# Optimization experiments

Hardware: AMD Instinct MI355X
Metric: run time of the kernel (lower is better)

Reference implementation:

```python
import jax, jax.numpy as jnp
import numpy as np

N = 30000      # nodes
E = 480000     # directed edges (before self loops)
G = 64         # graphs in batch
L = 20         # padded token-list length per node feature
D = 32         # embedding_dim
S = 64         # scalar_feature_count
H, C = 4, 128  # conv1 heads / hidden_channels
TOT = S + 5 * D  # 224
EPS_LN = 1e-5


def setup_inputs() -> dict:
    key = jax.random.key(0)
    ks = jax.random.split(key, 24)
    f32 = jnp.float32
    rn = lambda k, shp: jax.random.normal(k, shp, dtype=f32) * 0.05
    inp = {}
    inp["x_scalar"] = jax.random.normal(ks[0], (N, S), dtype=f32)
    inp["x_opcode"] = jax.random.randint(ks[1], (N, L), 0, 512)
    inp["x_source"] = jax.random.randint(ks[2], (N, L), 0, 256)
    inp["x_sink"] = jax.random.randint(ks[3], (N, L), 0, 256)
    inp["x_string_manip"] = jax.random.randint(ks[4], (N, L), 0, 128)
    inp["x_payload"] = jax.random.randint(ks[5], (N, L), 0, 256)
    inp["edge_index"] = jax.random.randint(ks[6], (2, E), 0, N)
    inp["batch"] = jnp.sort(jax.random.randint(ks[7], (N,), 0, G))
    inp["emb_opcode"] = rn(ks[8], (512, D))
    inp["emb_source"] = rn(ks[9], (256, D))
    inp["emb_sink"] = rn(ks[10], (256, D))
    inp["emb_string"] = rn(ks[11], (128, D))
    inp["emb_payload"] = rn(ks[12], (256, D))
    inp["ln_scale"] = jnp.ones((TOT,), f32)
    inp["ln_bias"] = jnp.zeros((TOT,), f32)
    inp["W1"] = rn(ks[13], (TOT, H * C))
    inp["att_src1"] = rn(ks[14], (H, C))
    inp["att_dst1"] = rn(ks[15], (H, C))
    inp["b1"] = jnp.zeros((H * C,), f32)
    inp["W2"] = rn(ks[16], (H * C, C))
    inp["att_src2"] = rn(ks[17], (1, C))
    inp["att_dst2"] = rn(ks[18], (1, C))
    inp["b2"] = jnp.zeros((C,), f32)
    return inp


def masked_pool(table, idx):
    # padding_idx=0 masked mean over the list dim
    emb = table[idx]                                    # [N, L, D]
    mask = (idx != 0).astype(emb.dtype)[..., None]      # [N, L, 1]
    return (emb * mask).sum(1) / (mask.sum(1) + 1e-9)   # [N, D]


def layer_norm(x, scale, bias):
    mu = x.mean(-1, keepdims=True)
    var = jnp.mean((x - mu) ** 2, -1, keepdims=True)
    return (x - mu) * jax.lax.rsqrt(var + EPS_LN) * scale + bias


def gat_layer(x, src, dst, W, a_src, a_dst, bias, n):
    # PyG GATConv (eval mode, concat=True, negative_slope=0.2)
    heads, c = a_src.shape
    h = (x @ W).reshape(n, heads, c)                    # [N, H, C]
    s = (h * a_src).sum(-1)                             # [N, H]
    d = (h * a_dst).sum(-1)                             # [N, H]
    e = jax.nn.leaky_relu(s[src] + d[dst], 0.2)         # [E, H]
    m = jax.ops.segment_max(e, dst, num_segments=n)     # segment softmax over dst
    ex = jnp.exp(e - m[dst])
    den = jax.ops.segment_sum(ex, dst, num_segments=n)
    alpha = ex / den[dst]                               # [E, H]
    out = jax.ops.segment_sum(alpha[:, :, None] * h[src], dst, num_segments=n)
    return out.reshape(n, heads * c) + bias


def reference(x_scalar, x_opcode, x_source, x_sink, x_string_manip, x_payload,
              edge_index, batch,
              emb_opcode, emb_source, emb_sink, emb_string, emb_payload,
              ln_scale, ln_bias,
              W1, att_src1, att_dst1, b1,
              W2, att_src2, att_dst2, b2):
    n = x_scalar.shape[0]
    feats = jnp.concatenate([
        x_scalar,
        masked_pool(emb_opcode, x_opcode),
        masked_pool(emb_source, x_source),
        masked_pool(emb_sink, x_sink),
        masked_pool(emb_string, x_string_manip),
        masked_pool(emb_payload, x_payload),
    ], axis=1)
    x = layer_norm(feats, ln_scale, ln_bias)
    # PyG GATConv adds self loops by default
    loops = jnp.arange(n)
    src = jnp.concatenate([edge_index[0], loops])
    dst = jnp.concatenate([edge_index[1], loops])
    x = jax.nn.elu(gat_layer(x, src, dst, W1, att_src1, att_dst1, b1, n))
    x = jax.nn.elu(gat_layer(x, src, dst, W2, att_src2, att_dst2, b2, n))
    # global_max_pool over graphs
    return jax.ops.segment_max(x, batch, num_segments=G)
```

## Files before the change

kernel.cpp:

```cpp
#include <hip/hip_runtime.h>
#include <hip/hip_bf16.h>
#include <math.h>

#define N_NODES 30000
#define M_PAD   30080
#define N_EDGES 480000
#define N_GRAPH 64
#define L_TOK   20
#define D_EMB   32
#define S_SCAL  64
#define TOT     224
#define H1      4
#define C1      128
#define F1      512
#define F2      128
#define E_TOT   (N_EDGES + N_NODES)

typedef __attribute__((ext_vector_type(8))) short bf16x8;
typedef __attribute__((ext_vector_type(4))) float f32x4;

__device__ __forceinline__ unsigned short f2b(float f) {
    unsigned u = __float_as_uint(f);
    u += 0x7FFFu + ((u >> 16) & 1u);
    return (unsigned short)(u >> 16);
}
__device__ __forceinline__ float b2f(unsigned short h) {
    return __uint_as_float(((unsigned)h) << 16);
}
__device__ __forceinline__ float blo(unsigned u) { return __uint_as_float(u << 16); }
__device__ __forceinline__ float bhi(unsigned u) { return __uint_as_float(u & 0xFFFF0000u); }

__device__ __forceinline__ void gload_lds16(const void* g, void* l) {
    __builtin_amdgcn_global_load_lds(
        (const __attribute__((address_space(1))) unsigned int*)g,
        (__attribute__((address_space(3))) unsigned int*)l, 16, 0, 0);
}

__global__ void init_all(int* deg, float* s1, float* d1, float* s2, float* d2) {
    int i = blockIdx.x * blockDim.x + threadIdx.x;
    if (i < N_NODES) {
        deg[i] = 1;
        s2[i] = 0.f; d2[i] = 0.f;
        float4 z = make_float4(0.f, 0.f, 0.f, 0.f);
        *reinterpret_cast<float4*>(&s1[i * 4]) = z;
        *reinterpret_cast<float4*>(&d1[i * 4]) = z;
    }
}

__global__ void add_deg(const int* __restrict__ ei, int* deg) {
    int e = blockIdx.x * blockDim.x + threadIdx.x;
    if (e < N_EDGES) atomicAdd(&deg[ei[N_EDGES + e]], 1);
}

#define SCAN_PER 30
__global__ void scan_deg(const int* __restrict__ deg, int* __restrict__ rowptr,
                         int* __restrict__ cursor) {
    int t = threadIdx.x, lane = t & 63, wid = t >> 6;
    int base = t * SCAN_PER;
    int v[SCAN_PER];
    int lsum = 0;
    #pragma unroll
    for (int i = 0; i < SCAN_PER; ++i) {
        int ii = base + i;
        int d = (ii < N_NODES) ? deg[ii] : 0;
        v[i] = lsum;
        lsum += d;
    }
    int incl = lsum;
    #pragma unroll
    for (int off = 1; off < 64; off <<= 1) {
        int u = __shfl_up(incl, off);
        if (lane >= off) incl += u;
    }
    __shared__ int wsum[16], woff[16];
    if (lane == 63) wsum[wid] = incl;
    __syncthreads();
    if (t == 0) {
        int run = 0;
        #pragma unroll
        for (int w = 0; w < 16; ++w) { woff[w] = run; run += wsum[w]; }
        rowptr[N_NODES] = run;
    }
    __syncthreads();
    int texcl = woff[wid] + (incl - lsum);
    #pragma unroll
    for (int i = 0; i < SCAN_PER; ++i) {
        int ii = base + i;
        if (ii < N_NODES) { int p = texcl + v[i]; rowptr[ii] = p; cursor[ii] = p; }
    }
}

__global__ void scatter_edges(const int* __restrict__ ei, int* cursor, int* csr_src) {
    int e = blockIdx.x * blockDim.x + threadIdx.x;
    if (e < N_EDGES) {
        int src = ei[e], dst = ei[N_EDGES + e];
        int pos = atomicAdd(&cursor[dst], 1);
        csr_src[pos] = src;
    } else if (e < E_TOT) {
        int n = e - N_EDGES;
        int pos = atomicAdd(&cursor[n], 1);
        csr_src[pos] = n;
    }
}

__global__ void transpose_cast2(const float* __restrict__ Wa, unsigned short* __restrict__ WaT,
                                const float* __restrict__ Wb, unsigned short* __restrict__ WbT) {
    __shared__ float tile[32][33];
    int bid = blockIdx.x;
    const float* W; unsigned short* WT; int K, N, kb, nb;
    if (bid < (TOT / 32) * (F1 / 32)) {
        W = Wa; WT = WaT; K = TOT; N = F1;
        kb = (bid % (TOT / 32)) * 32; nb = (bid / (TOT / 32)) * 32;
    } else {
        bid -= (TOT / 32) * (F1 / 32);
        W = Wb; WT = WbT; K = F1; N = F2;
        kb = (bid % (F1 / 32)) * 32; nb = (bid / (F1 / 32)) * 32;
    }
    int t = threadIdx.x;
    int r = t >> 3, c4 = (t & 7) * 4;
    float4 v = *reinterpret_cast<const float4*>(&W[(size_t)(kb + r) * N + nb + c4]);
    tile[r][c4 + 0] = v.x; tile[r][c4 + 1] = v.y;
    tile[r][c4 + 2] = v.z; tile[r][c4 + 3] = v.w;
    __syncthreads();
    ushort4 o;
    o.x = f2b(tile[c4 + 0][r]); o.y = f2b(tile[c4 + 1][r]);
    o.z = f2b(tile[c4 + 2][r]); o.w = f2b(tile[c4 + 3][r]);
    *reinterpret_cast<ushort4*>(&WT[(size_t)(nb + r) * K + kb + c4]) = o;
}

__global__ void feat_ln(const float* __restrict__ xs,
                        const int* __restrict__ xo, const int* __restrict__ xsrc,
                        const int* __restrict__ xsink, const int* __restrict__ xstr,
                        const int* __restrict__ xpay,
                        const float* __restrict__ eo, const float* __restrict__ es,
                        const float* __restrict__ ek, const float* __restrict__ eg,
                        const float* __restrict__ ep,
                        const float* __restrict__ lns, const float* __restrict__ lnb,
                        unsigned short* __restrict__ x0) {
    int node = blockIdx.x * 4 + (threadIdx.x >> 6);
    if (node >= N_NODES) return;
    int lane = threadIdx.x & 63;
    int c = lane * 4;
    float f0 = 0.f, f1 = 0.f, f2 = 0.f, f3 = 0.f;
    if (lane < 16) {
        float4 v = *reinterpret_cast<const float4*>(&xs[(size_t)node * S_SCAL + c]);
        f0 = v.x; f1 = v.y; f2 = v.z; f3 = v.w;
    } else if (lane < 56) {
        int t = c - S_SCAL;
        int ti = t >> 5, dim = t & 31;
        const int* idx; const float* emb;
        switch (ti) {
            case 0: idx = xo;   emb = eo; break;
            case 1: idx = xsrc; emb = es; break;
            case 2: idx = xsink;emb = ek; break;
            case 3: idx = xstr; emb = eg; break;
            default:idx = xpay; emb = ep; break;
        }
        float a0 = 0.f, a1 = 0.f, a2 = 0.f, a3 = 0.f, cnt = 0.f;
        #pragma unroll
        for (int l = 0; l < L_TOK; ++l) {
            int id = idx[node * L_TOK + l];
            if (id != 0) {
                float4 e = *reinterpret_cast<const float4*>(&emb[id * D_EMB + dim]);
                a0 += e.x; a1 += e.y; a2 += e.z; a3 += e.w; cnt += 1.f;
            }
        }
        float r = 1.f / (cnt + 1e-9f);
        f0 = a0 * r; f1 = a1 * r; f2 = a2 * r; f3 = a3 * r;
    }
    float s = f0 + f1 + f2 + f3;
    float q = f0 * f0 + f1 * f1 + f2 * f2 + f3 * f3;
    #pragma unroll
    for (int off = 32; off; off >>= 1) {
        s += __shfl_xor(s, off);
        q += __shfl_xor(q, off);
    }
    float mu = s * (1.f / (float)TOT);
    float var = q * (1.f / (float)TOT) - mu * mu;
    float rs = rsqrtf(var + 1e-5f);
    if (lane < 56) {
        float4 sc = *reinterpret_cast<const float4*>(&lns[c]);
        float4 bi = *reinterpret_cast<const float4*>(&lnb[c]);
        ushort4 o;
        o.x = f2b((f0 - mu) * rs * sc.x + bi.x);
        o.y = f2b((f1 - mu) * rs * sc.y + bi.y);
        o.z = f2b((f2 - mu) * rs * sc.z + bi.z);
        o.w = f2b((f3 - mu) * rs * sc.w + bi.w);
        *reinterpret_cast<ushort4*>(&x0[(size_t)node * TOT + c]) = o;
    }
}

__global__ void gemm_bf16(const unsigned short* __restrict__ A,
                          const unsigned short* __restrict__ BT,
                          unsigned short* __restrict__ C, int M, int N, int K,
                          const float* __restrict__ asrc, const float* __restrict__ adst,
                          float* __restrict__ sOut, float* __restrict__ dOut, int H) {
    __shared__ unsigned short As[128 * 32];
    __shared__ unsigned short Bs[128 * 32];
    int tid = threadIdx.x;
    int w = tid >> 6, lane = tid & 63;
    int l15 = lane & 15, kb = lane >> 4;
    int wr = w >> 1, wc = w & 1;
    int bm = blockIdx.x * 128, bn = blockIdx.y * 128;
    f32x4 acc[4][4] = {};
    int lrow = lane >> 2, lslot = lane & 3;

    for (int k0 = 0; k0 < K; k0 += 32) {
        #pragma unroll
        for (int j = 0; j < 2; ++j) {
            int rbase = w * 16 + j * 64;
            int row = rbase + lrow;
            int scol = (lslot ^ (row & 3)) * 8;
            gload_lds16(&A[(size_t)(bm + row) * K + k0 + scol], &As[rbase * 32]);
            gload_lds16(&BT[(size_t)(bn + row) * K + k0 + scol], &Bs[rbase * 32]);
        }
        __syncthreads();
        bf16x8 af[4], bf[4];
        #pragma unroll
        for (int m = 0; m < 4; ++m) {
            int row = wr * 64 + m * 16 + l15;
            af[m] = *reinterpret_cast<const bf16x8*>(&As[row * 32 + (kb ^ (row & 3)) * 8]);
        }
        #pragma unroll
        for (int n = 0; n < 4; ++n) {
            int row = wc * 64 + n * 16 + l15;
            bf[n] = *reinterpret_cast<const bf16x8*>(&Bs[row * 32 + (kb ^ (row & 3)) * 8]);
        }
        #pragma unroll
        for (int m = 0; m < 4; ++m)
            #pragma unroll
            for (int n = 0; n < 4; ++n)
                acc[m][n] = __builtin_amdgcn_mfma_f32_16x16x32_bf16(af[m], bf[n], acc[m][n], 0, 0, 0);
        __syncthreads();
    }
    #pragma unroll
    for (int m = 0; m < 4; ++m) {
        #pragma unroll
        for (int r = 0; r < 4; ++r) {
            int row = bm + wr * 64 + m * 16 + kb * 4 + r;
            if (row < M) {
                #pragma unroll
                for (int n = 0; n < 4; ++n)
                    C[(size_t)row * N + bn + wc * 64 + n * 16 + l15] = f2b(acc[m][n][r]);
            }
        }
    }
    {
        float a_s[4], a_d[4];
        #pragma unroll
        for (int n = 0; n < 4; ++n) {
            a_s[n] = asrc[bn + wc * 64 + n * 16 + l15];
            a_d[n] = adst[bn + wc * 64 + n * 16 + l15];
        }
        int head = bn / (N / H);
        #pragma unroll
        for (int m = 0; m < 4; ++m) {
            #pragma unroll
            for (int r = 0; r < 4; ++r) {
                float ps = acc[m][0][r] * a_s[0] + acc[m][1][r] * a_s[1]
                         + acc[m][2][r] * a_s[2] + acc[m][3][r] * a_s[3];
                float pd = acc[m][0][r] * a_d[0] + acc[m][1][r] * a_d[1]
                         + acc[m][2][r] * a_d[2] + acc[m][3][r] * a_d[3];
                #pragma unroll
                for (int off = 8; off >= 1; off >>= 1) {
                    ps += __shfl_xor(ps, off);
                    pd += __shfl_xor(pd, off);
                }
                if (l15 == 0) {
                    int row = bm + wr * 64 + m * 16 + kb * 4 + r;
                    if (row < M) {
                        atomicAdd(&sOut[row * H + head], ps);
                        atomicAdd(&dOut[row * H + head], pd);
                    }
                }
            }
        }
    }
}

#define ACC8(v, a) \
    acc[0] += (a) * blo((v).x); acc[1] += (a) * bhi((v).x); \
    acc[2] += (a) * blo((v).y); acc[3] += (a) * bhi((v).y); \
    acc[4] += (a) * blo((v).z); acc[5] += (a) * bhi((v).z); \
    acc[6] += (a) * blo((v).w); acc[7] += (a) * bhi((v).w);

__global__ void gat1_aggregate(const unsigned short* __restrict__ h1, const float* __restrict__ s1,
                               const float* __restrict__ d1, const int* __restrict__ rowptr,
                               const int* __restrict__ csr, const float* __restrict__ b1,
                               unsigned short* __restrict__ x1) {
    int n = blockIdx.x, tid = threadIdx.x;
    int wave = tid >> 6, lane = tid & 63;
    int head = lane >> 4;
    int r0 = rowptr[n], deg = rowptr[n + 1] - r0;
    __shared__ float alpha_sh[H1][68];
    __shared__ int src_sh[64];
    __shared__ float d_n[H1];
    __shared__ float red[3][512];
    if (tid < H1) d_n[tid] = d1[n * H1 + tid];
    __syncthreads();
    float dnw = d_n[wave];
    const uint4* h1u4 = (const uint4*)h1;
    float acc[8] = {};

    auto gather = [&](int cnt) {
        int iA = wave, iB = wave + 4, iC = wave + 8, iD = wave + 12;
        bool hA = iA < cnt, hB = iB < cnt, hC = iC < cnt, hD = iD < cnt;
        int s; float aA, aB, aC, aD; uint4 vA, vB, vC, vD;
        if (hA) { s = __builtin_amdgcn_readfirstlane(src_sh[iA]); aA = alpha_sh[head][iA]; vA = h1u4[(size_t)s * 64 + lane]; }
        if (hB) { s = __builtin_amdgcn_readfirstlane(src_sh[iB]); aB = alpha_sh[head][iB]; vB = h1u4[(size_t)s * 64 + lane]; }
        if (hC) { s = __builtin_amdgcn_readfirstlane(src_sh[iC]); aC = alpha_sh[head][iC]; vC = h1u4[(size_t)s * 64 + lane]; }
        if (hD) { s = __builtin_amdgcn_readfirstlane(src_sh[iD]); aD = alpha_sh[head][iD]; vD = h1u4[(size_t)s * 64 + lane]; }
        while (hA) {
            {
                uint4 v = vA; float a = aA;
                iA += 16; hA = iA < cnt;
                if (hA) { s = __builtin_amdgcn_readfirstlane(src_sh[iA]); aA = alpha_sh[head][iA]; vA = h1u4[(size_t)s * 64 + lane]; }
                ACC8(v, a)
            }
            if (hB) {
                uint4 v = vB; float a = aB;
                iB += 16; hB = iB < cnt;
                if (hB) { s = __builtin_amdgcn_readfirstlane(src_sh[iB]); aB = alpha_sh[head][iB]; vB = h1u4[(size_t)s * 64 + lane]; }
                ACC8(v, a)
            }
            if (hC) {
                uint4 v = vC; float a = aC;
                iC += 16; hC = iC < cnt;
                if (hC) { s = __builtin_amdgcn_readfirstlane(src_sh[iC]); aC = alpha_sh[head][iC]; vC = h1u4[(size_t)s * 64 + lane]; }
                ACC8(v, a)
            }
            if (hD) {
                uint4 v = vD; float a = aD;
                iD += 16; hD = iD < cnt;
                if (hD) { s = __builtin_amdgcn_readfirstlane(src_sh[iD]); aD = alpha_sh[head][iD]; vD = h1u4[(size_t)s * 64 + lane]; }
                ACC8(v, a)
            }
        }
    };

    if (deg <= 64) {
        float e = -1e30f;
        if (lane < deg) {
            int src = csr[r0 + lane];
            if (wave == 0) src_sh[lane] = src;
            float ev = s1[src * H1 + wave] + dnw;
            e = (ev >= 0.f) ? ev : 0.2f * ev;
        }
        float m = e;
        #pragma unroll
        for (int off = 32; off; off >>= 1) m = fmaxf(m, __shfl_xor(m, off));
        float ex = (lane < deg) ? __expf(e - m) : 0.f;
        float den = ex;
        #pragma unroll
        for (int off = 32; off; off >>= 1) den += __shfl_xor(den, off);
        alpha_sh[wave][lane] = ex / den;
        __syncthreads();
        gather(deg);
    } else {
        float m = -1e30f;
        for (int i = lane; i < deg; i += 64) {
            int src = csr[r0 + i];
            float e = s1[src * H1 + wave] + dnw;
            e = (e >= 0.f) ? e : 0.2f * e;
            m = fmaxf(m, e);
        }
        #pragma unroll
        for (int off = 32; off; off >>= 1) m = fmaxf(m, __shfl_xor(m, off));
        float den = 0.f;
        for (int i = lane; i < deg; i += 64) {
            int src = csr[r0 + i];
            float e = s1[src * H1 + wave] + dnw;
            e = (e >= 0.f) ? e : 0.2f * e;
            den += __expf(e - m);
        }
        #pragma unroll
        for (int off = 32; off; off >>= 1) den += __shfl_xor(den, off);
        float invw = 1.f / den;
        for (int c0 = 0; c0 < deg; c0 += 64) {
            __syncthreads();
            int i = c0 + lane;
            if (i < deg) {
                int src = csr[r0 + i];
                if (wave == 0) src_sh[lane] = src;
                float e = s1[src * H1 + wave] + dnw;
                e = (e >= 0.f) ? e : 0.2f * e;
                alpha_sh[wave][lane] = __expf(e - m) * invw;
            }
            __syncthreads();
            gather(min(64, deg - c0));
        }
    }
    if (wave > 0) {
        *reinterpret_cast<float4*>(&red[wave - 1][lane * 4]) =
            make_float4(acc[0], acc[1], acc[2], acc[3]);
        *reinterpret_cast<float4*>(&red[wave - 1][256 + lane * 4]) =
            make_float4(acc[4], acc[5], acc[6], acc[7]);
    }
    __syncthreads();
    if (wave == 0) {
        #pragma unroll
        for (int w = 0; w < 3; ++w) {
            float4 p = *reinterpret_cast<float4*>(&red[w][lane * 4]);
            float4 q = *reinterpret_cast<float4*>(&red[w][256 + lane * 4]);
            acc[0] += p.x; acc[1] += p.y; acc[2] += p.z; acc[3] += p.w;
            acc[4] += q.x; acc[5] += q.y; acc[6] += q.z; acc[7] += q.w;
        }
        float4 b0 = *reinterpret_cast<const float4*>(&b1[lane * 8]);
        float4 b4 = *reinterpret_cast<const float4*>(&b1[lane * 8 + 4]);
        float v0 = acc[0] + b0.x; v0 = (v0 > 0.f) ? v0 : expm1f(v0);
        float v1 = acc[1] + b0.y; v1 = (v1 > 0.f) ? v1 : expm1f(v1);
        float v2 = acc[2] + b0.z; v2 = (v2 > 0.f) ? v2 : expm1f(v2);
        float v3 = acc[3] + b0.w; v3 = (v3 > 0.f) ? v3 : expm1f(v3);
        float v4 = acc[4] + b4.x; v4 = (v4 > 0.f) ? v4 : expm1f(v4);
        float v5 = acc[5] + b4.y; v5 = (v5 > 0.f) ? v5 : expm1f(v5);
        float v6 = acc[6] + b4.z; v6 = (v6 > 0.f) ? v6 : expm1f(v6);
        float v7 = acc[7] + b4.w; v7 = (v7 > 0.f) ? v7 : expm1f(v7);
        uint4 pk;
        pk.x = (unsigned)f2b(v0) | ((unsigned)f2b(v1) << 16);
        pk.y = (unsigned)f2b(v2) | ((unsigned)f2b(v3) << 16);
        pk.z = (unsigned)f2b(v4) | ((unsigned)f2b(v5) << 16);
        pk.w = (unsigned)f2b(v6) | ((unsigned)f2b(v7) << 16);
        ((uint4*)x1)[(size_t)n * 64 + lane] = pk;
    }
}

__global__ void gat2_node(const unsigned short* __restrict__ h2, const float* __restrict__ s2,
                          const float* __restrict__ d2, const int* __restrict__ rowptr,
                          const int* __restrict__ csr, const float* __restrict__ b2,
                          float* __restrict__ h2act) {
    int n = blockIdx.x, tid = threadIdx.x;
    int wid = tid >> 6, lane = tid & 63;
    int grp = tid >> 4, l16 = tid & 15;
    int r0 = rowptr[n], deg = rowptr[n + 1] - r0;
    __shared__ float alpha_sh[128];
    __shared__ int src_sh[128];
    __shared__ float rA[2], rB[2];
    __shared__ float red[8][128];
    float dn = d2[n];
    const uint4* h2u4 = (const uint4*)h2;
    float acc[8] = {};

    auto gather = [&](int cnt) {
        int iA = grp, iB = grp + 8, iC = grp + 16, iD = grp + 24;
        bool hA = iA < cnt, hB = iB < cnt, hC = iC < cnt, hD = iD < cnt;
        int s; float aA, aB, aC, aD; uint4 vA, vB, vC, vD;
        if (hA) { s = src_sh[iA]; aA = alpha_sh[iA]; vA = h2u4[(size_t)s * 16 + l16]; }
        if (hB) { s = src_sh[iB]; aB = alpha_sh[iB]; vB = h2u4[(size_t)s * 16 + l16]; }
        if (hC) { s = src_sh[iC]; aC = alpha_sh[iC]; vC = h2u4[(size_t)s * 16 + l16]; }
        if (hD) { s = src_sh[iD]; aD = alpha_sh[iD]; vD = h2u4[(size_t)s * 16 + l16]; }
        while (hA) {
            {
                uint4 v = vA; float a = aA;
                iA += 32; hA = iA < cnt;
                if (hA) { s = src_sh[iA]; aA = alpha_sh[iA]; vA = h2u4[(size_t)s * 16 + l16]; }
                ACC8(v, a)
            }
            if (hB) {
                uint4 v = vB; float a = aB;
                iB += 32; hB = iB < cnt;
                if (hB) { s = src_sh[iB]; aB = alpha_sh[iB]; vB = h2u4[(size_t)s * 16 + l16]; }
                ACC8(v, a)
            }
            if (hC) {
                uint4 v = vC; float a = aC;
                iC += 32; hC = iC < cnt;
                if (hC) { s = src_sh[iC]; aC = alpha_sh[iC]; vC = h2u4[(size_t)s * 16 + l16]; }
                ACC8(v, a)
            }
            if (hD) {
                uint4 v = vD; float a = aD;
                iD += 32; hD = iD < cnt;
                if (hD) { s = src_sh[iD]; aD = alpha_sh[iD]; vD = h2u4[(size_t)s * 16 + l16]; }
                ACC8(v, a)
            }
        }
    };

    if (deg <= 128) {
        float e = -1e30f;
        if (tid < deg) {
            int src = csr[r0 + tid];
            src_sh[tid] = src;
            float ev = s2[src] + dn;
            e = (ev >= 0.f) ? ev : 0.2f * ev;
        }
        float m = e;
        #pragma unroll
        for (int off = 32; off; off >>= 1) m = fmaxf(m, __shfl_xor(m, off));
        if (lane == 0) rA[wid] = m;
        __syncthreads();
        m = fmaxf(rA[0], rA[1]);
        float ex = (tid < deg) ? __expf(e - m) : 0.f;
        float den = ex;
        #pragma unroll
        for (int off = 32; off; off >>= 1) den += __shfl_xor(den, off);
        if (lane == 0) rB[wid] = den;
        __syncthreads();
        den = rB[0] + rB[1];
        alpha_sh[tid] = ex / den;
        __syncthreads();
        gather(deg);
    } else {
        float m = -1e30f;
        for (int i = tid; i < deg; i += 128) {
            float e = s2[csr[r0 + i]] + dn; e = (e >= 0.f) ? e : 0.2f * e;
            m = fmaxf(m, e);
        }
        #pragma unroll
        for (int off = 32; off; off >>= 1) m = fmaxf(m, __shfl_xor(m, off));
        if (lane == 0) rA[wid] = m;
        __syncthreads();
        m = fmaxf(rA[0], rA[1]);
        float den = 0.f;
        for (int i = tid; i < deg; i += 128) {
            float e = s2[csr[r0 + i]] + dn; e = (e >= 0.f) ? e : 0.2f * e;
            den += __expf(e - m);
        }
        #pragma unroll
        for (int off = 32; off; off >>= 1) den += __shfl_xor(den, off);
        if (lane == 0) rB[wid] = den;
        __syncthreads();
        den = rB[0] + rB[1];
        float inv = 1.f / den;
        for (int c0 = 0; c0 < deg; c0 += 128) {
            __syncthreads();
            int i = c0 + tid;
            if (i < deg) {
                int src = csr[r0 + i];
                src_sh[tid] = src;
                float e = s2[src] + dn; e = (e >= 0.f) ? e : 0.2f * e;
                alpha_sh[tid] = __expf(e - m) * inv;
            }
            __syncthreads();
            gather(min(128, deg - c0));
        }
    }
    *reinterpret_cast<float4*>(&red[grp][l16 * 4]) =
        make_float4(acc[0], acc[1], acc[2], acc[3]);
    *reinterpret_cast<float4*>(&red[grp][64 + l16 * 4]) =
        make_float4(acc[4], acc[5], acc[6], acc[7]);
    __syncthreads();
    {
        int pos = tid;
        int ch = (pos < 64) ? ((pos >> 2) * 8 + (pos & 3))
                            : (((pos - 64) >> 2) * 8 + 4 + (pos & 3));
        float s = red[0][pos] + red[1][pos] + red[2][pos] + red[3][pos]
                + red[4][pos] + red[5][pos] + red[6][pos] + red[7][pos] + b2[ch];
        s = (s > 0.f) ? s : expm1f(s);
        h2act[(size_t)n * F2 + ch] = s;
    }
}

__global__ void graph_pool(const float* __restrict__ h2act, const int* __restrict__ batch,
                           float* __restrict__ out) {
    int gph = blockIdx.x;
    int tid = threadIdx.x;
    __shared__ int se[2];
    __shared__ float red[128];
    if (tid < 2) {
        int target = gph + tid;
        int lo = 0, hi = N_NODES;
        while (lo < hi) { int mid = (lo + hi) >> 1; if (batch[mid] < target) lo = mid + 1; else hi = mid; }
        se[tid] = lo;
    }
    __syncthreads();
    int start = se[0], end = se[1];
    int ch = tid & 127, noff = tid >> 7;
    float m = -INFINITY;
    for (int i = start + noff; i < end; i += 2)
        m = fmaxf(m, h2act[(size_t)i * F2 + ch]);
    if (noff == 1) red[ch] = m;
    __syncthreads();
    if (noff == 0) out[gph * F2 + ch] = fmaxf(m, red[ch]);
}

extern "C" void kernel_launch(void* const* d_in, const int* in_sizes, int n_in,
                              void* d_out, int out_size, void* d_ws, size_t ws_size,
                              hipStream_t stream) {
    const float* x_scalar = (const float*)d_in[0];
    const int*   x_opcode = (const int*)d_in[1];
    const int*   x_source = (const int*)d_in[2];
    const int*   x_sink   = (const int*)d_in[3];
    const int*   x_string = (const int*)d_in[4];
    const int*   x_payload= (const int*)d_in[5];
    const int*   edge_idx = (const int*)d_in[6];
    const int*   batch    = (const int*)d_in[7];
    const float* emb_op   = (const float*)d_in[8];
    const float* emb_src  = (const float*)d_in[9];
    const float* emb_snk  = (const float*)d_in[10];
    const float* emb_str  = (const float*)d_in[11];
    const float* emb_pay  = (const float*)d_in[12];
    const float* ln_scale = (const float*)d_in[13];
    const float* ln_bias  = (const float*)d_in[14];
    const float* W1       = (const float*)d_in[15];
    const float* att_src1 = (const float*)d_in[16];
    const float* att_dst1 = (const float*)d_in[17];
    const float* b1       = (const float*)d_in[18];
    const float* W2       = (const float*)d_in[19];
    const float* att_src2 = (const float*)d_in[20];
    const float* att_dst2 = (const float*)d_in[21];
    const float* b2       = (const float*)d_in[22];
    float* out = (float*)d_out;

    unsigned short* x0  = (unsigned short*)d_ws;
    unsigned short* h1  = x0 + (size_t)M_PAD * TOT;
    unsigned short* x1  = h1 + (size_t)M_PAD * F1;
    unsigned short* h2  = x1 + (size_t)M_PAD * F1;
    unsigned short* W1T = h2 + (size_t)M_PAD * F2;
    unsigned short* W2T = W1T + (size_t)F1 * TOT;
    float* s1 = (float*)(W2T + (size_t)F2 * F1);
    float* d1 = s1 + (size_t)N_NODES * H1;
    float* s2 = d1 + (size_t)N_NODES * H1;
    float* d2 = s2 + N_NODES;
    int* rowptr = (int*)(d2 + N_NODES);
    int* cursor = rowptr + (N_NODES + 1);
    int* csr    = cursor + (N_NODES + 1);
    float* h2act = (float*)x1;

    init_all<<<(N_NODES + 255) / 256, 256, 0, stream>>>(cursor, s1, d1, s2, d2);
    add_deg<<<(N_EDGES + 255) / 256, 256, 0, stream>>>(edge_idx, cursor);
    scan_deg<<<1, 1024, 0, stream>>>(cursor, rowptr, cursor);
    scatter_edges<<<(E_TOT + 255) / 256, 256, 0, stream>>>(edge_idx, cursor, csr);

    transpose_cast2<<<(TOT / 32) * (F1 / 32) + (F1 / 32) * (F2 / 32), 256, 0, stream>>>(
        W1, W1T, W2, W2T);

    feat_ln<<<(N_NODES + 3) / 4, 256, 0, stream>>>(x_scalar, x_opcode, x_source, x_sink,
                                                   x_string, x_payload, emb_op, emb_src,
                                                   emb_snk, emb_str, emb_pay, ln_scale,
                                                   ln_bias, x0);

    dim3 g1(M_PAD / 128, F1 / 128);
    gemm_bf16<<<g1, 256, 0, stream>>>(x0, W1T, h1, N_NODES, F1, TOT,
                                      att_src1, att_dst1, s1, d1, H1);
    gat1_aggregate<<<N_NODES, 256, 0, stream>>>(h1, s1, d1, rowptr, csr, b1, x1);

    dim3 g2(M_PAD / 128, F2 / 128);
    gemm_bf16<<<g2, 256, 0, stream>>>(x1, W2T, h2, N_NODES, F2, F1,
                                      att_src2, att_dst2, s2, d2, 1);

    gat2_node<<<N_NODES, 128, 0, stream>>>(h2, s2, d2, rowptr, csr, b2, h2act);
    graph_pool<<<N_GRAPH, 256, 0, stream>>>(h2act, batch, out);
}
```

Baseline: 342.8 us.

## Split GAT aggregation into per-edge softmax and column-sliced gather kernels

```diff
diff --git a/kernel.cpp b/kernel.cpp
--- a/kernel.cpp
+++ b/kernel.cpp
@@ -24,11 +24,10 @@
     u += 0x7FFFu + ((u >> 16) & 1u);
     return (unsigned short)(u >> 16);
 }
-__device__ __forceinline__ float b2f(unsigned short h) {
-    return __uint_as_float(((unsigned)h) << 16);
-}
 __device__ __forceinline__ float blo(unsigned u) { return __uint_as_float(u << 16); }
 __device__ __forceinline__ float bhi(unsigned u) { return __uint_as_float(u & 0xFFFF0000u); }
+__device__ __forceinline__ float lrelu(float x) { return (x >= 0.f) ? x : 0.2f * x; }
+__device__ __forceinline__ float elu(float x) { return (x > 0.f) ? x : expm1f(x); }
 
 __device__ __forceinline__ void gload_lds16(const void* g, void* l) {
     __builtin_amdgcn_global_load_lds(
@@ -278,276 +277,209 @@
     }
 }
 
-#define ACC8(v, a) \
-    acc[0] += (a) * blo((v).x); acc[1] += (a) * bhi((v).x); \
-    acc[2] += (a) * blo((v).y); acc[3] += (a) * bhi((v).y); \
-    acc[4] += (a) * blo((v).z); acc[5] += (a) * bhi((v).z); \
-    acc[6] += (a) * blo((v).w); acc[7] += (a) * bhi((v).w);
-
-__global__ void gat1_aggregate(const unsigned short* __restrict__ h1, const float* __restrict__ s1,
-                               const float* __restrict__ d1, const int* __restrict__ rowptr,
-                               const int* __restrict__ csr, const float* __restrict__ b1,
-                               unsigned short* __restrict__ x1) {
-    int n = blockIdx.x, tid = threadIdx.x;
-    int wave = tid >> 6, lane = tid & 63;
-    int head = lane >> 4;
+__global__ void gat1_softmax(const float* __restrict__ s1, const float* __restrict__ d1,
+                             const int* __restrict__ rowptr, const int* __restrict__ csr,
+                             float* __restrict__ alphaE) {
+    int node = blockIdx.x * 4 + (threadIdx.x >> 6);
+    if (node >= N_NODES) return;
+    int lane = threadIdx.x & 63;
+    int r0 = rowptr[node], deg = rowptr[node + 1] - r0;
+    float4 dn = *reinterpret_cast<const float4*>(&d1[node * 4]);
+    if (deg <= 64) {
+        float e0 = -1e30f, e1 = -1e30f, e2 = -1e30f, e3 = -1e30f;
+        bool act = lane < deg;
+        if (act) {
+            int src = csr[r0 + lane];
+            float4 sv = *reinterpret_cast<const float4*>(&s1[src * 4]);
+            e0 = lrelu(sv.x + dn.x); e1 = lrelu(sv.y + dn.y);
+            e2 = lrelu(sv.z + dn.z); e3 = lrelu(sv.w + dn.w);
+        }
+        float m0 = e0, m1 = e1, m2 = e2, m3 = e3;
+        #pragma unroll
+        for (int off = 32; off; off >>= 1) {
+            m0 = fmaxf(m0, __shfl_xor(m0, off)); m1 = fmaxf(m1, __shfl_xor(m1, off));
+            m2 = fmaxf(m2, __shfl_xor(m2, off)); m3 = fmaxf(m3, __shfl_xor(m3, off));
+        }
+        float x0 = act ? __expf(e0 - m0) : 0.f, x1 = act ? __expf(e1 - m1) : 0.f;
+        float x2 = act ? __expf(e2 - m2) : 0.f, x3 = act ? __expf(e3 - m3) : 0.f;
+        float q0 = x0, q1 = x1, q2 = x2, q3 = x3;
+        #pragma unroll
+        for (int off = 32; off; off >>= 1) {
+            q0 += __shfl_xor(q0, off); q1 += __shfl_xor(q1, off);
+            q2 += __shfl_xor(q2, off); q3 += __shfl_xor(q3, off);
+        }
+        if (act) {
+            float4 a = make_float4(x0 / q0, x1 / q1, x2 / q2, x3 / q3);
+            *reinterpret_cast<float4*>(&alphaE[(size_t)(r0 + lane) * 4]) = a;
+        }
+    } else {
+        float m0 = -1e30f, m1 = -1e30f, m2 = -1e30f, m3 = -1e30f;
+        for (int i = lane; i < deg; i += 64) {
+            int src = csr[r0 + i];
+            float4 sv = *reinterpret_cast<const float4*>(&s1[src * 4]);
+            m0 = fmaxf(m0, lrelu(sv.x + dn.x)); m1 = fmaxf(m1, lrelu(sv.y + dn.y));
+            m2 = fmaxf(m2, lrelu(sv.z + dn.z)); m3 = fmaxf(m3, lrelu(sv.w + dn.w));
+        }
+        #pragma unroll
+        for (int off = 32; off; off >>= 1) {
+            m0 = fmaxf(m0, __shfl_xor(m0, off)); m1 = fmaxf(m1, __shfl_xor(m1, off));
+            m2 = fmaxf(m2, __shfl_xor(m2, off)); m3 = fmaxf(m3, __shfl_xor(m3, off));
+        }
+        float q0 = 0.f, q1 = 0.f, q2 = 0.f, q3 = 0.f;
+        for (int i = lane; i < deg; i += 64) {
+            int src = csr[r0 + i];
+            float4 sv = *reinterpret_cast<const float4*>(&s1[src * 4]);
+            q0 += __expf(lrelu(sv.x + dn.x) - m0); q1 += __expf(lrelu(sv.y + dn.y) - m1);
+            q2 += __expf(lrelu(sv.z + dn.z) - m2); q3 += __expf(lrelu(sv.w + dn.w) - m3);
+        }
+        #pragma unroll
+        for (int off = 32; off; off >>= 1) {
+            q0 += __shfl_xor(q0, off); q1 += __shfl_xor(q1, off);
+            q2 += __shfl_xor(q2, off); q3 += __shfl_xor(q3, off);
+        }
+        float i0 = 1.f / q0, i1 = 1.f / q1, i2 = 1.f / q2, i3 = 1.f / q3;
+        for (int i = lane; i < deg; i += 64) {
+            int src = csr[r0 + i];
+            float4 sv = *reinterpret_cast<const float4*>(&s1[src * 4]);
+            float4 a = make_float4(__expf(lrelu(sv.x + dn.x) - m0) * i0,
+                                   __expf(lrelu(sv.y + dn.y) - m1) * i1,
+                                   __expf(lrelu(sv.z + dn.z) - m2) * i2,
+                                   __expf(lrelu(sv.w + dn.w) - m3) * i3);
+            *reinterpret_cast<float4*>(&alphaE[(size_t)(r0 + i) * 4]) = a;
+        }
+    }
+}
+
+__global__ void gat1_gather(const unsigned short* __restrict__ h1,
+                            const float* __restrict__ alphaE,
+                            const int* __restrict__ rowptr, const int* __restrict__ csr,
+                            const float* __restrict__ b1, unsigned short* __restrict__ x1) {
+    int s = blockIdx.x & 7, nb = blockIdx.x >> 3;
+    int n = nb * 4 + (threadIdx.x >> 6);
+    if (n >= N_NODES) return;
+    int lane = threadIdx.x & 63, grp = lane >> 4, l16 = lane & 15;
     int r0 = rowptr[n], deg = rowptr[n + 1] - r0;
-    __shared__ float alpha_sh[H1][68];
-    __shared__ int src_sh[64];
-    __shared__ float d_n[H1];
-    __shared__ float red[3][512];
-    if (tid < H1) d_n[tid] = d1[n * H1 + tid];
-    __syncthreads();
-    float dnw = d_n[wave];
-    const uint4* h1u4 = (const uint4*)h1;
-    float acc[8] = {};
-
-    auto gather = [&](int cnt) {
-        int iA = wave, iB = wave + 4, iC = wave + 8, iD = wave + 12;
-        bool hA = iA < cnt, hB = iB < cnt, hC = iC < cnt, hD = iD < cnt;
-        int s; float aA, aB, aC, aD; uint4 vA, vB, vC, vD;
-        if (hA) { s = __builtin_amdgcn_readfirstlane(src_sh[iA]); aA = alpha_sh[head][iA]; vA = h1u4[(size_t)s * 64 + lane]; }
-        if (hB) { s = __builtin_amdgcn_readfirstlane(src_sh[iB]); aB = alpha_sh[head][iB]; vB = h1u4[(size_t)s * 64 + lane]; }
-        if (hC) { s = __builtin_amdgcn_readfirstlane(src_sh[iC]); aC = alpha_sh[head][iC]; vC = h1u4[(size_t)s * 64 + lane]; }
-        if (hD) { s = __builtin_amdgcn_readfirstlane(src_sh[iD]); aD = alpha_sh[head][iD]; vD = h1u4[(size_t)s * 64 + lane]; }
-        while (hA) {
-            {
-                uint4 v = vA; float a = aA;
-                iA += 16; hA = iA < cnt;
-                if (hA) { s = __builtin_amdgcn_readfirstlane(src_sh[iA]); aA = alpha_sh[head][iA]; vA = h1u4[(size_t)s * 64 + lane]; }
-                ACC8(v, a)
-            }
-            if (hB) {
-                uint4 v = vB; float a = aB;
-                iB += 16; hB = iB < cnt;
-                if (hB) { s = __builtin_amdgcn_readfirstlane(src_sh[iB]); aB = alpha_sh[head][iB]; vB = h1u4[(size_t)s * 64 + lane]; }
-                ACC8(v, a)
-            }
-            if (hC) {
-                uint4 v = vC; float a = aC;
-                iC += 16; hC = iC < cnt;
-                if (hC) { s = __builtin_amdgcn_readfirstlane(src_sh[iC]); aC = alpha_sh[head][iC]; vC = h1u4[(size_t)s * 64 + lane]; }
-                ACC8(v, a)
-            }
-            if (hD) {
-                uint4 v = vD; float a = aD;
-                iD += 16; hD = iD < cnt;
-                if (hD) { s = __builtin_amdgcn_readfirstlane(src_sh[iD]); aD = alpha_sh[head][iD]; vD = h1u4[(size_t)s * 64 + lane]; }
-                ACC8(v, a)
-            }
-        }
-    };
-
+    int head = s >> 1;
+    const uint2* h1u2 = (const uint2*)h1;
+    float a0 = 0.f, a1 = 0.f, a2 = 0.f, a3 = 0.f;
+    int base = (size_t)0;
+    (void)base;
+    int iA = grp, iB = grp + 4;
+    bool hA = iA < deg, hB = iB < deg;
+    int sA, sB; float aA, aB; uint2 vA, vB;
+    if (hA) { sA = csr[r0 + iA]; aA = alphaE[(size_t)(r0 + iA) * 4 + head]; vA = h1u2[(size_t)sA * 128 + s * 16 + l16]; }
+    if (hB) { sB = csr[r0 + iB]; aB = alphaE[(size_t)(r0 + iB) * 4 + head]; vB = h1u2[(size_t)sB * 128 + s * 16 + l16]; }
+    while (hA) {
+        {
+            uint2 v = vA; float a = aA;
+            iA += 8; hA = iA < deg;
+            if (hA) { sA = csr[r0 + iA]; aA = alphaE[(size_t)(r0 + iA) * 4 + head]; vA = h1u2[(size_t)sA * 128 + s * 16 + l16]; }
+            a0 += a * blo(v.x); a1 += a * bhi(v.x);
+            a2 += a * blo(v.y); a3 += a * bhi(v.y);
+        }
+        if (hB) {
+            uint2 v = vB; float a = aB;
+            iB += 8; hB = iB < deg;
+            if (hB) { sB = csr[r0 + iB]; aB = alphaE[(size_t)(r0 + iB) * 4 + head]; vB = h1u2[(size_t)sB * 128 + s * 16 + l16]; }
+            a0 += a * blo(v.x); a1 += a * bhi(v.x);
+            a2 += a * blo(v.y); a3 += a * bhi(v.y);
+        }
+    }
+    #pragma unroll
+    for (int off = 16; off <= 32; off <<= 1) {
+        a0 += __shfl_xor(a0, off); a1 += __shfl_xor(a1, off);
+        a2 += __shfl_xor(a2, off); a3 += __shfl_xor(a3, off);
+    }
+    if (lane < 16) {
+        int c = s * 64 + l16 * 4;
+        float4 bv = *reinterpret_cast<const float4*>(&b1[c]);
+        float v0 = elu(a0 + bv.x), v1 = elu(a1 + bv.y);
+        float v2 = elu(a2 + bv.z), v3 = elu(a3 + bv.w);
+        uint2 pk;
+        pk.x = (unsigned)f2b(v0) | ((unsigned)f2b(v1) << 16);
+        pk.y = (unsigned)f2b(v2) | ((unsigned)f2b(v3) << 16);
+        ((uint2*)x1)[(size_t)n * 128 + s * 16 + l16] = pk;
+    }
+}
+
+__global__ void gat2_softmax(const float* __restrict__ s2, const float* __restrict__ d2,
+                             const int* __restrict__ rowptr, const int* __restrict__ csr,
+                             float* __restrict__ alpha2E) {
+    int node = blockIdx.x * 4 + (threadIdx.x >> 6);
+    if (node >= N_NODES) return;
+    int lane = threadIdx.x & 63;
+    int r0 = rowptr[node], deg = rowptr[node + 1] - r0;
+    float dn = d2[node];
     if (deg <= 64) {
         float e = -1e30f;
-        if (lane < deg) {
-            int src = csr[r0 + lane];
-            if (wave == 0) src_sh[lane] = src;
-            float ev = s1[src * H1 + wave] + dnw;
-            e = (ev >= 0.f) ? ev : 0.2f * ev;
-        }
+        bool act = lane < deg;
+        if (act) e = lrelu(s2[csr[r0 + lane]] + dn);
         float m = e;
         #pragma unroll
         for (int off = 32; off; off >>= 1) m = fmaxf(m, __shfl_xor(m, off));
-        float ex = (lane < deg) ? __expf(e - m) : 0.f;
-        float den = ex;
-        #pragma unroll
-        for (int off = 32; off; off >>= 1) den += __shfl_xor(den, off);
-        alpha_sh[wave][lane] = ex / den;
-        __syncthreads();
-        gather(deg);
+        float x = act ? __expf(e - m) : 0.f;
+        float q = x;
+        #pragma unroll
+        for (int off = 32; off; off >>= 1) q += __shfl_xor(q, off);
+        if (act) alpha2E[r0 + lane] = x / q;
     } else {
         float m = -1e30f;
-        for (int i = lane; i < deg; i += 64) {
-            int src = csr[r0 + i];
-            float e = s1[src * H1 + wave] + dnw;
-            e = (e >= 0.f) ? e : 0.2f * e;
-            m = fmaxf(m, e);
-        }
+        for (int i = lane; i < deg; i += 64) m = fmaxf(m, lrelu(s2[csr[r0 + i]] + dn));
         #pragma unroll
         for (int off = 32; off; off >>= 1) m = fmaxf(m, __shfl_xor(m, off));
-        float den = 0.f;
-        for (int i = lane; i < deg; i += 64) {
-            int src = csr[r0 + i];
-            float e = s1[src * H1 + wave] + dnw;
-            e = (e >= 0.f) ? e : 0.2f * e;
-            den += __expf(e - m);
-        }
-        #pragma unroll
-        for (int off = 32; off; off >>= 1) den += __shfl_xor(den, off);
-        float invw = 1.f / den;
-        for (int c0 = 0; c0 < deg; c0 += 64) {
-            __syncthreads();
-            int i = c0 + lane;
-            if (i < deg) {
-                int src = csr[r0 + i];
-                if (wave == 0) src_sh[lane] = src;
-                float e = s1[src * H1 + wave] + dnw;
-                e = (e >= 0.f) ? e : 0.2f * e;
-                alpha_sh[wave][lane] = __expf(e - m) * invw;
-            }
-            __syncthreads();
-            gather(min(64, deg - c0));
-        }
-    }
-    if (wave > 0) {
-        *reinterpret_cast<float4*>(&red[wave - 1][lane * 4]) =
-            make_float4(acc[0], acc[1], acc[2], acc[3]);
-        *reinterpret_cast<float4*>(&red[wave - 1][256 + lane * 4]) =
-            make_float4(acc[4], acc[5], acc[6], acc[7]);
-    }
-    __syncthreads();
-    if (wave == 0) {
-        #pragma unroll
-        for (int w = 0; w < 3; ++w) {
-            float4 p = *reinterpret_cast<float4*>(&red[w][lane * 4]);
-            float4 q = *reinterpret_cast<float4*>(&red[w][256 + lane * 4]);
-            acc[0] += p.x; acc[1] += p.y; acc[2] += p.z; acc[3] += p.w;
-            acc[4] += q.x; acc[5] += q.y; acc[6] += q.z; acc[7] += q.w;
-        }
-        float4 b0 = *reinterpret_cast<const float4*>(&b1[lane * 8]);
-        float4 b4 = *reinterpret_cast<const float4*>(&b1[lane * 8 + 4]);
-        float v0 = acc[0] + b0.x; v0 = (v0 > 0.f) ? v0 : expm1f(v0);
-        float v1 = acc[1] + b0.y; v1 = (v1 > 0.f) ? v1 : expm1f(v1);
-        float v2 = acc[2] + b0.z; v2 = (v2 > 0.f) ? v2 : expm1f(v2);
-        float v3 = acc[3] + b0.w; v3 = (v3 > 0.f) ? v3 : expm1f(v3);
-        float v4 = acc[4] + b4.x; v4 = (v4 > 0.f) ? v4 : expm1f(v4);
-        float v5 = acc[5] + b4.y; v5 = (v5 > 0.f) ? v5 : expm1f(v5);
-        float v6 = acc[6] + b4.z; v6 = (v6 > 0.f) ? v6 : expm1f(v6);
-        float v7 = acc[7] + b4.w; v7 = (v7 > 0.f) ? v7 : expm1f(v7);
-        uint4 pk;
-        pk.x = (unsigned)f2b(v0) | ((unsigned)f2b(v1) << 16);
-        pk.y = (unsigned)f2b(v2) | ((unsigned)f2b(v3) << 16);
-        pk.z = (unsigned)f2b(v4) | ((unsigned)f2b(v5) << 16);
-        pk.w = (unsigned)f2b(v6) | ((unsigned)f2b(v7) << 16);
-        ((uint4*)x1)[(size_t)n * 64 + lane] = pk;
-    }
-}
-
-__global__ void gat2_node(const unsigned short* __restrict__ h2, const float* __restrict__ s2,
-                          const float* __restrict__ d2, const int* __restrict__ rowptr,
-                          const int* __restrict__ csr, const float* __restrict__ b2,
-                          float* __restrict__ h2act) {
-    int n = blockIdx.x, tid = threadIdx.x;
-    int wid = tid >> 6, lane = tid & 63;
-    int grp = tid >> 4, l16 = tid & 15;
+        float q = 0.f;
+        for (int i = lane; i < deg; i += 64) q += __expf(lrelu(s2[csr[r0 + i]] + dn) - m);
+        #pragma unroll
+        for (int off = 32; off; off >>= 1) q += __shfl_xor(q, off);
+        float inv = 1.f / q;
+        for (int i = lane; i < deg; i += 64)
+            alpha2E[r0 + i] = __expf(lrelu(s2[csr[r0 + i]] + dn) - m) * inv;
+    }
+}
+
+__global__ void gat2_gather(const unsigned short* __restrict__ h2,
+                            const float* __restrict__ alpha2E,
+                            const int* __restrict__ rowptr, const int* __restrict__ csr,
+                            const float* __restrict__ b2, float* __restrict__ h2act) {
+    int s = blockIdx.x & 1, nb = blockIdx.x >> 1;
+    int n = nb * 4 + (threadIdx.x >> 6);
+    if (n >= N_NODES) return;
+    int lane = threadIdx.x & 63, grp = lane >> 4, l16 = lane & 15;
     int r0 = rowptr[n], deg = rowptr[n + 1] - r0;
-    __shared__ float alpha_sh[128];
-    __shared__ int src_sh[128];
-    __shared__ float rA[2], rB[2];
-    __shared__ float red[8][128];
-    float dn = d2[n];
-    const uint4* h2u4 = (const uint4*)h2;
-    float acc[8] = {};
-
-    auto gather = [&](int cnt) {
-        int iA = grp, iB = grp + 8, iC = grp + 16, iD = grp + 24;
-        bool hA = iA < cnt, hB = iB < cnt, hC = iC < cnt, hD = iD < cnt;
-        int s; float aA, aB, aC, aD; uint4 vA, vB, vC, vD;
-        if (hA) { s = src_sh[iA]; aA = alpha_sh[iA]; vA = h2u4[(size_t)s * 16 + l16]; }
-        if (hB) { s = src_sh[iB]; aB = alpha_sh[iB]; vB = h2u4[(size_t)s * 16 + l16]; }
-        if (hC) { s = src_sh[iC]; aC = alpha_sh[iC]; vC = h2u4[(size_t)s * 16 + l16]; }
-        if (hD) { s = src_sh[iD]; aD = alpha_sh[iD]; vD = h2u4[(size_t)s * 16 + l16]; }
-        while (hA) {
-            {
-                uint4 v = vA; float a = aA;
-                iA += 32; hA = iA < cnt;
-                if (hA) { s = src_sh[iA]; aA = alpha_sh[iA]; vA = h2u4[(size_t)s * 16 + l16]; }
-                ACC8(v, a)
-            }
-            if (hB) {
-                uint4 v = vB; float a = aB;
-                iB += 32; hB = iB < cnt;
-                if (hB) { s = src_sh[iB]; aB = alpha_sh[iB]; vB = h2u4[(size_t)s * 16 + l16]; }
-                ACC8(v, a)
-            }
-            if (hC) {
-                uint4 v = vC; float a = aC;
-                iC += 32; hC = iC < cnt;
-                if (hC) { s = src_sh[iC]; aC = alpha_sh[iC]; vC = h2u4[(size_t)s * 16 + l16]; }
-                ACC8(v, a)
-            }
-            if (hD) {
-                uint4 v = vD; float a = aD;
-                iD += 32; hD = iD < cnt;
-                if (hD) { s = src_sh[iD]; aD = alpha_sh[iD]; vD = h2u4[(size_t)s * 16 + l16]; }
-                ACC8(v, a)
-            }
-        }
-    };
-
-    if (deg <= 128) {
-        float e = -1e30f;
-        if (tid < deg) {
-            int src = csr[r0 + tid];
-            src_sh[tid] = src;
-            float ev = s2[src] + dn;
-            e = (ev >= 0.f) ? ev : 0.2f * ev;
-        }
-        float m = e;
-        #pragma unroll
-        for (int off = 32; off; off >>= 1) m = fmaxf(m, __shfl_xor(m, off));
-        if (lane == 0) rA[wid] = m;
-        __syncthreads();
-        m = fmaxf(rA[0], rA[1]);
-        float ex = (tid < deg) ? __expf(e - m) : 0.f;
-        float den = ex;
-        #pragma unroll
-        for (int off = 32; off; off >>= 1) den += __shfl_xor(den, off);
-        if (lane == 0) rB[wid] = den;
-        __syncthreads();
-        den = rB[0] + rB[1];
-        alpha_sh[tid] = ex / den;
-        __syncthreads();
-        gather(deg);
-    } else {
-        float m = -1e30f;
-        for (int i = tid; i < deg; i += 128) {
-            float e = s2[csr[r0 + i]] + dn; e = (e >= 0.f) ? e : 0.2f * e;
-            m = fmaxf(m, e);
-        }
-        #pragma unroll
-        for (int off = 32; off; off >>= 1) m = fmaxf(m, __shfl_xor(m, off));
-        if (lane == 0) rA[wid] = m;
-        __syncthreads();
-        m = fmaxf(rA[0], rA[1]);
-        float den = 0.f;
-        for (int i = tid; i < deg; i += 128) {
-            float e = s2[csr[r0 + i]] + dn; e = (e >= 0.f) ? e : 0.2f * e;
-            den += __expf(e - m);
-        }
-        #pragma unroll
-        for (int off = 32; off; off >>= 1) den += __shfl_xor(den, off);
-        if (lane == 0) rB[wid] = den;
-        __syncthreads();
-        den = rB[0] + rB[1];
-        float inv = 1.f / den;
-        for (int c0 = 0; c0 < deg; c0 += 128) {
-            __syncthreads();
-            int i = c0 + tid;
-            if (i < deg) {
-                int src = csr[r0 + i];
-                src_sh[tid] = src;
-                float e = s2[src] + dn; e = (e >= 0.f) ? e : 0.2f * e;
-                alpha_sh[tid] = __expf(e - m) * inv;
-            }
-            __syncthreads();
-            gather(min(128, deg - c0));
-        }
-    }
-    *reinterpret_cast<float4*>(&red[grp][l16 * 4]) =
-        make_float4(acc[0], acc[1], acc[2], acc[3]);
-    *reinterpret_cast<float4*>(&red[grp][64 + l16 * 4]) =
-        make_float4(acc[4], acc[5], acc[6], acc[7]);
-    __syncthreads();
-    {
-        int pos = tid;
-        int ch = (pos < 64) ? ((pos >> 2) * 8 + (pos & 3))
-                            : (((pos - 64) >> 2) * 8 + 4 + (pos & 3));
-        float s = red[0][pos] + red[1][pos] + red[2][pos] + red[3][pos]
-                + red[4][pos] + red[5][pos] + red[6][pos] + red[7][pos] + b2[ch];
-        s = (s > 0.f) ? s : expm1f(s);
-        h2act[(size_t)n * F2 + ch] = s;
+    const uint2* h2u2 = (const uint2*)h2;
+    float a0 = 0.f, a1 = 0.f, a2 = 0.f, a3 = 0.f;
+    int iA = grp, iB = grp + 4;
+    bool hA = iA < deg, hB = iB < deg;
+    int sA, sB; float aA, aB; uint2 vA, vB;
+    if (hA) { sA = csr[r0 + iA]; aA = alpha2E[r0 + iA]; vA = h2u2[(size_t)sA * 32 + s * 16 + l16]; }
+    if (hB) { sB = csr[r0 + iB]; aB = alpha2E[r0 + iB]; vB = h2u2[(size_t)sB * 32 + s * 16 + l16]; }
+    while (hA) {
+        {
+            uint2 v = vA; float a = aA;
+            iA += 8; hA = iA < deg;
+            if (hA) { sA = csr[r0 + iA]; aA = alpha2E[r0 + iA]; vA = h2u2[(size_t)sA * 32 + s * 16 + l16]; }
+            a0 += a * blo(v.x); a1 += a * bhi(v.x);
+            a2 += a * blo(v.y); a3 += a * bhi(v.y);
+        }
+        if (hB) {
+            uint2 v = vB; float a = aB;
+            iB += 8; hB = iB < deg;
+            if (hB) { sB = csr[r0 + iB]; aB = alpha2E[r0 + iB]; vB = h2u2[(size_t)sB * 32 + s * 16 + l16]; }
+            a0 += a * blo(v.x); a1 += a * bhi(v.x);
+            a2 += a * blo(v.y); a3 += a * bhi(v.y);
+        }
+    }
+    #pragma unroll
+    for (int off = 16; off <= 32; off <<= 1) {
+        a0 += __shfl_xor(a0, off); a1 += __shfl_xor(a1, off);
+        a2 += __shfl_xor(a2, off); a3 += __shfl_xor(a3, off);
+    }
+    if (lane < 16) {
+        int c = s * 64 + l16 * 4;
+        float4 bv = *reinterpret_cast<const float4*>(&b2[c]);
+        float4 o = make_float4(elu(a0 + bv.x), elu(a1 + bv.y),
+                               elu(a2 + bv.z), elu(a3 + bv.w));
+        *reinterpret_cast<float4*>(&h2act[(size_t)n * F2 + c]) = o;
     }
 }
 
@@ -615,6 +547,8 @@
     int* rowptr = (int*)(d2 + N_NODES);
     int* cursor = rowptr + (N_NODES + 1);
     int* csr    = cursor + (N_NODES + 1);
+    float* alphaE  = (float*)(csr + E_TOT);
+    float* alpha2E = alphaE + (size_t)E_TOT * 4;
     float* h2act = (float*)x1;
 
     init_all<<<(N_NODES + 255) / 256, 256, 0, stream>>>(cursor, s1, d1, s2, d2);
@@ -633,12 +567,14 @@
     dim3 g1(M_PAD / 128, F1 / 128);
     gemm_bf16<<<g1, 256, 0, stream>>>(x0, W1T, h1, N_NODES, F1, TOT,
                                       att_src1, att_dst1, s1, d1, H1);
-    gat1_aggregate<<<N_NODES, 256, 0, stream>>>(h1, s1, d1, rowptr, csr, b1, x1);
+    gat1_softmax<<<(N_NODES + 3) / 4, 256, 0, stream>>>(s1, d1, rowptr, csr, alphaE);
+    gat1_gather<<<((N_NODES + 3) / 4) * 8, 256, 0, stream>>>(h1, alphaE, rowptr, csr, b1, x1);
 
     dim3 g2(M_PAD / 128, F2 / 128);
     gemm_bf16<<<g2, 256, 0, stream>>>(x1, W2T, h2, N_NODES, F2, F1,
                                       att_src2, att_dst2, s2, d2, 1);
-
-    gat2_node<<<N_NODES, 128, 0, stream>>>(h2, s2, d2, rowptr, csr, b2, h2act);
+    gat2_softmax<<<(N_NODES + 3) / 4, 256, 0, stream>>>(s2, d2, rowptr, csr, alpha2E);
+    gat2_gather<<<((N_NODES + 3) / 4) * 2, 256, 0, stream>>>(h2, alpha2E, rowptr, csr, b2, h2act);
+
     graph_pool<<<N_GRAPH, 256, 0, stream>>>(h2act, batch, out);
 }
```

Result: slower. 423.1 us (+23.4%).
